# Kernel tuning notes

Hardware: AMD Instinct MI355X
Metric: run time of the kernel (lower is better)

Reference implementation:

```python
import jax, jax.numpy as jnp
import numpy as np

V = 100000      # num nodes
E = 600000      # num edges (even: first half in-edges, second half out-edges)
D_IN = 128
D_OUT = 128
NREL2 = 100     # num_rel * 2
BN_EPS = 1e-5


def ccorr(a, b):
    # circular correlation along last dim: irfft(conj(rfft(a)) * rfft(b), n=d)
    d = a.shape[-1]
    return jnp.fft.irfft(jnp.conj(jnp.fft.rfft(a)) * jnp.fft.rfft(b), n=d).astype(a.dtype)


def setup_inputs() -> dict:
    key = jax.random.key(0)
    ks = jax.random.split(key, 12)
    return {
        "x": jax.random.normal(ks[0], (V, D_IN), dtype=jnp.float32),
        "rel_repr": jax.random.normal(ks[1], (NREL2, D_IN), dtype=jnp.float32),
        "edge_norm": jax.random.uniform(ks[2], (E,), dtype=jnp.float32),
        "in_w": jax.random.normal(ks[3], (D_IN, D_OUT), dtype=jnp.float32) * 0.05,
        "out_w": jax.random.normal(ks[4], (D_IN, D_OUT), dtype=jnp.float32) * 0.05,
        "loop_w": jax.random.normal(ks[5], (D_IN, D_OUT), dtype=jnp.float32) * 0.05,
        "w_rel": jax.random.normal(ks[6], (D_IN, D_OUT), dtype=jnp.float32) * 0.05,
        "loop_rel": jax.random.normal(ks[7], (1, D_IN), dtype=jnp.float32),
        "bias": jnp.zeros((D_OUT,), dtype=jnp.float32),
        "bn_gamma": jnp.ones((D_OUT,), dtype=jnp.float32),
        "bn_beta": jnp.zeros((D_OUT,), dtype=jnp.float32),
        "edge_src": jax.random.randint(ks[8], (E,), 0, V, dtype=jnp.int32),
        "edge_dst": jax.random.randint(ks[9], (E,), 0, V, dtype=jnp.int32),
        "edge_type": jax.random.randint(ks[10], (E,), 0, NREL2, dtype=jnp.int32),
    }


def reference(x, rel_repr, edge_norm, in_w, out_w, loop_w, w_rel, loop_rel,
              bias, bn_gamma, bn_beta, edge_src, edge_dst, edge_type):
    rel = rel_repr  # rel_wt is None (num_base=-1)
    # gather src features per edge and compose with relation embedding (corr)
    edge_data = ccorr(x[edge_src], rel[edge_type])             # [E, D_IN]
    half = edge_data.shape[0] // 2
    msg = jnp.concatenate(
        [edge_data[:half] @ in_w, edge_data[half:] @ out_w], axis=0
    ) * edge_norm[:, None]                                     # [E, D_OUT]
    # scatter-sum into destination nodes
    agg = jax.ops.segment_sum(msg, edge_dst, num_segments=V)   # [V, D_OUT]
    # self-loop term
    loop = ccorr(x, jnp.broadcast_to(loop_rel, x.shape)) @ loop_w
    h = (agg + loop) / 3.0 + bias
    # BatchNorm1d (training mode: batch stats, biased variance)
    mean = h.mean(axis=0)
    var = h.var(axis=0)
    h = (h - mean) * jax.lax.rsqrt(var + BN_EPS) * bn_gamma + bn_beta
    # act is identity; ltr=True -> project relations
    return h, rel @ w_rel
```

## Files before the change

### kernel.cpp

```cpp
#include <hip/hip_runtime.h>
#include <hip/hip_bf16.h>

#define D 128
constexpr int V_N    = 100000;
constexpr int E_N    = 600000;
constexpr int HALF_E = E_N / 2;
constexpr int NREL2  = 100;
constexpr int NBUCK  = 2 * NREL2;
constexpr float BN_EPS_F = 1e-5f;

constexpr int CHUNK  = 4096;
constexpr int NCHUNK = (E_N + CHUNK - 1) / CHUNK;

typedef short bf16x8  __attribute__((ext_vector_type(8)));
typedef float f32x16  __attribute__((ext_vector_type(16)));
typedef float f32x4v  __attribute__((ext_vector_type(4)));

constexpr size_t M_RSV    = 201ull * D * D * 4;
constexpr size_t M_OFF    = 0;
constexpr size_t HIST_OFF = 201ull * D * D * 2;
constexpr size_t COFF_OFF = HIST_OFF + (size_t)NBUCK * NCHUNK * 4;
constexpr size_t SS_OFF   = M_RSV;
constexpr size_t SD_OFF   = SS_OFF + (size_t)E_N * 4;
constexpr size_t SN_OFF   = SD_OFF + (size_t)E_N * 4;
constexpr size_t ZERO_OFF = SN_OFF + (size_t)E_N * 4;
constexpr size_t CNT_OFF  = ZERO_OFF;
constexpr size_t CS_OFF   = ZERO_OFF + 1024;
constexpr size_t CQ_OFF   = CS_OFF + 512;
constexpr size_t ZERO_BYTES = 2048;
constexpr size_t ST_OFF   = ZERO_OFF + ZERO_BYTES;

constexpr size_t MT_BYTES  = 201ull * D * D * 2;
constexpr size_t P_SS_OFF  = MT_BYTES;
constexpr size_t P_SD_OFF  = P_SS_OFF + (size_t)E_N * 4;
constexpr size_t P_SN_OFF  = P_SD_OFF + (size_t)E_N * 4;
constexpr size_t P_AGG_OFF = P_SN_OFF + (size_t)E_N * 4;
constexpr size_t AGG_BYTES = (size_t)V_N * D * 2;
constexpr size_t P_HIST_OFF = P_AGG_OFF;
constexpr size_t P_COFF_OFF = P_HIST_OFF + (size_t)NBUCK * NCHUNK * 4;
constexpr size_t P_CS_OFF  = P_AGG_OFF + AGG_BYTES;
constexpr size_t P_CQ_OFF  = P_CS_OFF + 512;
constexpr size_t P_CNT_OFF = P_CQ_OFF + 512;
constexpr size_t P_ST_OFF  = P_CNT_OFF + 1024;
constexpr size_t WS_NEED_PK = P_ST_OFF + 1024;

__device__ inline unsigned short f2bf(float f) {
    __hip_bfloat16 h = __float2bfloat16(f);
    return __builtin_bit_cast(unsigned short, h);
}
__device__ inline float bf2f(unsigned short u) {
    return __uint_as_float(((unsigned)u) << 16);
}

__device__ inline int bucket_of(int e, const int* __restrict__ etype) {
    return etype[e] + (e < HALF_E ? 0 : NREL2);
}

__global__ __launch_bounds__(256) void k_hist_chunk(const int* __restrict__ etype,
                                                    int* __restrict__ hist) {
    __shared__ int h[NBUCK];
    for (int i = threadIdx.x; i < NBUCK; i += 256) h[i] = 0;
    __syncthreads();
    int c = blockIdx.x;
    int e0 = c * CHUNK;
#pragma unroll
    for (int r = 0; r < CHUNK / 256; r++) {
        int e = e0 + r * 256 + threadIdx.x;
        if (e < E_N) atomicAdd(&h[bucket_of(e, etype)], 1);
    }
    __syncthreads();
    for (int b = threadIdx.x; b < NBUCK; b += 256) hist[b * NCHUNK + c] = h[b];
}

__global__ void k_scan_bucket(const int* __restrict__ hist, int* __restrict__ chunkoff,
                              int* __restrict__ counts) {
    int b = blockIdx.x, lane = threadIdx.x;
    int acc = 0;
    for (int base = 0; base < NCHUNK; base += 64) {
        int c = base + lane;
        int v = (c < NCHUNK) ? hist[b * NCHUNK + c] : 0;
        int s = v;
#pragma unroll
        for (int off = 1; off < 64; off <<= 1) {
            int t = __shfl(s, lane - off, 64);
            if (lane >= off) s += t;
        }
        if (c < NCHUNK) chunkoff[b * NCHUNK + c] = acc + (s - v);
        acc += __shfl(s, 63, 64);
    }
    if (lane == 0) counts[b] = acc;
}

__global__ void k_scan(const int* __restrict__ counts, int* __restrict__ starts) {
    __shared__ int s[256];
    int i = threadIdx.x;
    int v = (i < NBUCK) ? counts[i] : 0;
    s[i] = v;
    __syncthreads();
    for (int off = 1; off < 256; off <<= 1) {
        int t = (i >= off) ? s[i - off] : 0;
        __syncthreads();
        s[i] += t;
        __syncthreads();
    }
    if (i < NBUCK) starts[i] = s[i] - v;
    if (i == 255) starts[NBUCK] = s[255];
}

__global__ __launch_bounds__(256) void k_scatter2(
    const int* __restrict__ src, const int* __restrict__ dst,
    const float* __restrict__ norm, const int* __restrict__ etype,
    const int* __restrict__ starts, const int* __restrict__ chunkoff,
    int* __restrict__ ssrc, int* __restrict__ sdst, float* __restrict__ snorm) {
    __shared__ int h[NBUCK];
    __shared__ int sbase[NBUCK];
    int c = blockIdx.x;
    for (int b = threadIdx.x; b < NBUCK; b += 256) {
        h[b] = 0;
        sbase[b] = starts[b] + chunkoff[b * NCHUNK + c];
    }
    __syncthreads();
    int e0 = c * CHUNK;
#pragma unroll
    for (int r = 0; r < CHUNK / 256; r++) {
        int e = e0 + r * 256 + threadIdx.x;
        if (e < E_N) {
            int b = bucket_of(e, etype);
            int rank = atomicAdd(&h[b], 1);
            int p = sbase[b] + rank;
            ssrc[p] = src[e]; sdst[p] = dst[e]; snorm[p] = norm[e];
        }
    }
}

__global__ void k_build_M(const float* __restrict__ rel, const float* __restrict__ in_w,
                          const float* __restrict__ out_w, const float* __restrict__ loop_rel,
                          const float* __restrict__ loop_w, ushort* __restrict__ MT) {
    extern __shared__ float smem[];
    float* sW = smem;
    float* sR = smem + D * D;
    int b = blockIdx.x;
    const float* r = (b < NREL2) ? rel + (size_t)b * D
                   : (b < NBUCK) ? rel + (size_t)(b - NREL2) * D : loop_rel;
    const float* W = (b < NREL2) ? in_w : (b < NBUCK) ? out_w : loop_w;
    for (int i = threadIdx.x; i < D * D; i += blockDim.x) sW[i] = W[i];
    for (int i = threadIdx.x; i < D; i += blockDim.x) { float v = r[i]; sR[i] = v; sR[i + D] = v; }
    __syncthreads();
    int o  = threadIdx.x & 127;
    int jg = threadIdx.x >> 7;
    ushort* MTb = MT + (size_t)b * (D * D);
    for (int pass = 0; pass < 4; pass++) {
        int jbase = jg * 64 + pass * 16;
        float acc[16];
#pragma unroll
        for (int t = 0; t < 16; t++) acc[t] = 0.f;
        for (int k = 0; k < D; k++) {
            float w = sW[k * D + o];
#pragma unroll
            for (int t = 0; t < 16; t++) acc[t] += sR[jbase + t + k] * w;
        }
#pragma unroll
        for (int t = 0; t < 16; t++) MTb[(size_t)o * D + jbase + t] = f2bf(acc[t]);
    }
}

__global__ void k_relw(const float* __restrict__ rel, const float* __restrict__ w_rel,
                       float* __restrict__ out2) {
    int rr = blockIdx.x, o = threadIdx.x;
    float acc = 0.f;
    for (int k = 0; k < D; k++) acc += rel[rr * D + k] * w_rel[k * D + o];
    out2[rr * D + o] = acc;
}

constexpr int BPB = 8;

__global__ __launch_bounds__(256) void k_edge_pk(
    const float* __restrict__ x, const ushort* __restrict__ MT,
    const int* __restrict__ starts, const int* __restrict__ ssrc,
    const int* __restrict__ sdst, const float* __restrict__ snorm,
    ushort* __restrict__ agg) {
    int wid  = threadIdx.x >> 6, lane = threadIdx.x & 63;
    int l31  = lane & 31, l5 = lane >> 5;
    int bucket = blockIdx.x / BPB;
    int sib    = (blockIdx.x % BPB) * 2 + (wid >> 1);
    int oh     = wid & 1;
    int bstart = starts[bucket], bend = starts[bucket + 1];
    const ushort* MTb = MT + (size_t)bucket * (D * D);
    int c0 = oh * 64 + 2 * l31;
    bf16x8 B0[8], B1[8];
#pragma unroll
    for (int kc = 0; kc < 8; kc++) {
        B0[kc] = *(const bf16x8*)&MTb[(size_t)c0 * D + kc * 16 + l5 * 8];
        B1[kc] = *(const bf16x8*)&MTb[(size_t)(c0 + 1) * D + kc * 16 + l5 * 8];
    }
    for (int tbase = bstart + sib * 32; tbase < bend; tbase += BPB * 2 * 32) {
        int nv = bend - tbase; if (nv > 32) nv = 32;
        int sr = ssrc[tbase + (l31 < nv ? l31 : 0)];
        const float* xr = x + (size_t)sr * D + l5 * 8;
        bf16x8 A[8];
#pragma unroll
        for (int kc = 0; kc < 8; kc++) {
            f32x4v v0 = *(const f32x4v*)(xr + kc * 16);
            f32x4v v1 = *(const f32x4v*)(xr + kc * 16 + 4);
            union { bf16x8 v; ushort u[8]; } t;
            t.u[0] = f2bf(v0[0]); t.u[1] = f2bf(v0[1]); t.u[2] = f2bf(v0[2]); t.u[3] = f2bf(v0[3]);
            t.u[4] = f2bf(v1[0]); t.u[5] = f2bf(v1[1]); t.u[6] = f2bf(v1[2]); t.u[7] = f2bf(v1[3]);
            A[kc] = t.v;
        }
        f32x16 C0, C1;
#pragma unroll
        for (int i = 0; i < 16; i++) { C0[i] = 0.f; C1[i] = 0.f; }
#pragma unroll
        for (int kc = 0; kc < 8; kc++) {
            C0 = __builtin_amdgcn_mfma_f32_32x32x16_bf16(A[kc], B0[kc], C0, 0, 0, 0);
            C1 = __builtin_amdgcn_mfma_f32_32x32x16_bf16(A[kc], B1[kc], C1, 0, 0, 0);
        }
#pragma unroll
        for (int r = 0; r < 16; r++) {
            int rw = (r & 3) + 8 * (r >> 2) + 4 * l5;
            if (rw < nv) {
                float nm = snorm[tbase + rw];
                int   dv = sdst[tbase + rw];
                union { ushort u[2]; unsigned int w; } p;
                p.u[0] = f2bf(C0[r] * nm);
                p.u[1] = f2bf(C1[r] * nm);
                ushort* ap = agg + (size_t)dv * D + c0;
                asm volatile("global_atomic_pk_add_bf16 %0, %1, off"
                             :: "v"(ap), "v"(p.w) : "memory");
            }
        }
    }
}

__global__ __launch_bounds__(256) void k_edge(
    const float* __restrict__ x, const ushort* __restrict__ MT,
    const int* __restrict__ starts, const int* __restrict__ ssrc,
    const int* __restrict__ sdst, const float* __restrict__ snorm,
    float* __restrict__ out) {
    int wid  = threadIdx.x >> 6, lane = threadIdx.x & 63;
    int l31  = lane & 31, l5 = lane >> 5;
    int bucket = blockIdx.x / BPB;
    int sib    = (blockIdx.x % BPB) * 2 + (wid >> 1);
    int oh     = wid & 1;
    int bstart = starts[bucket], bend = starts[bucket + 1];
    const ushort* MTb = MT + (size_t)bucket * (D * D);
    int ocol0 = oh * 64 + l31, ocol1 = oh * 64 + 32 + l31;
    bf16x8 B0[8], B1[8];
#pragma unroll
    for (int kc = 0; kc < 8; kc++) {
        B0[kc] = *(const bf16x8*)&MTb[(size_t)ocol0 * D + kc * 16 + l5 * 8];
        B1[kc] = *(const bf16x8*)&MTb[(size_t)ocol1 * D + kc * 16 + l5 * 8];
    }
    for (int tbase = bstart + sib * 32; tbase < bend; tbase += BPB * 2 * 32) {
        int nv = bend - tbase; if (nv > 32) nv = 32;
        int sr = ssrc[tbase + (l31 < nv ? l31 : 0)];
        const float* xr = x + (size_t)sr * D + l5 * 8;
        bf16x8 A[8];
#pragma unroll
        for (int kc = 0; kc < 8; kc++) {
            f32x4v v0 = *(const f32x4v*)(xr + kc * 16);
            f32x4v v1 = *(const f32x4v*)(xr + kc * 16 + 4);
            union { bf16x8 v; ushort u[8]; } t;
            t.u[0] = f2bf(v0[0]); t.u[1] = f2bf(v0[1]); t.u[2] = f2bf(v0[2]); t.u[3] = f2bf(v0[3]);
            t.u[4] = f2bf(v1[0]); t.u[5] = f2bf(v1[1]); t.u[6] = f2bf(v1[2]); t.u[7] = f2bf(v1[3]);
            A[kc] = t.v;
        }
        f32x16 C0, C1;
#pragma unroll
        for (int i = 0; i < 16; i++) { C0[i] = 0.f; C1[i] = 0.f; }
#pragma unroll
        for (int kc = 0; kc < 8; kc++) {
            C0 = __builtin_amdgcn_mfma_f32_32x32x16_bf16(A[kc], B0[kc], C0, 0, 0, 0);
            C1 = __builtin_amdgcn_mfma_f32_32x32x16_bf16(A[kc], B1[kc], C1, 0, 0, 0);
        }
#pragma unroll
        for (int r = 0; r < 16; r++) {
            int rw = (r & 3) + 8 * (r >> 2) + 4 * l5;
            if (rw < nv) {
                float nm = snorm[tbase + rw];
                int   dv = sdst[tbase + rw];
                float* op = out + (size_t)dv * D;
                atomicAdd(op + ocol0, C0[r] * nm);
                atomicAdd(op + ocol1, C1[r] * nm);
            }
        }
    }
}

constexpr int LOOP_GRID = 400;
__global__ __launch_bounds__(256) void k_loop_pk(
    const float* __restrict__ x, const ushort* __restrict__ MT,
    const float* __restrict__ bias, const ushort* __restrict__ agg,
    float* __restrict__ out, float* __restrict__ colsum, float* __restrict__ colsq) {
    int wid = threadIdx.x >> 6, lane = threadIdx.x & 63;
    int l31 = lane & 31, l5 = lane >> 5;
    int oh  = wid & 1;
    int strm = blockIdx.x * 2 + (wid >> 1);
    const int NSTR = LOOP_GRID * 2;
    const ushort* MTb = MT + (size_t)NBUCK * (D * D);
    int ocol0 = oh * 64 + l31, ocol1 = oh * 64 + 32 + l31;
    bf16x8 B0[8], B1[8];
#pragma unroll
    for (int kc = 0; kc < 8; kc++) {
        B0[kc] = *(const bf16x8*)&MTb[(size_t)ocol0 * D + kc * 16 + l5 * 8];
        B1[kc] = *(const bf16x8*)&MTb[(size_t)ocol1 * D + kc * 16 + l5 * 8];
    }
    float b0 = bias[ocol0], b1 = bias[ocol1];
    float ps0 = 0.f, pq0 = 0.f, ps1 = 0.f, pq1 = 0.f;
    const int NT = V_N / 32;
    for (int tile = strm; tile < NT; tile += NSTR) {
        int tbase = tile * 32;
        const float* xr = x + (size_t)(tbase + l31) * D + l5 * 8;
        bf16x8 A[8];
#pragma unroll
        for (int kc = 0; kc < 8; kc++) {
            f32x4v v0 = *(const f32x4v*)(xr + kc * 16);
            f32x4v v1 = *(const f32x4v*)(xr + kc * 16 + 4);
            union { bf16x8 v; ushort u[8]; } t;
            t.u[0] = f2bf(v0[0]); t.u[1] = f2bf(v0[1]); t.u[2] = f2bf(v0[2]); t.u[3] = f2bf(v0[3]);
            t.u[4] = f2bf(v1[0]); t.u[5] = f2bf(v1[1]); t.u[6] = f2bf(v1[2]); t.u[7] = f2bf(v1[3]);
            A[kc] = t.v;
        }
        f32x16 C0, C1;
#pragma unroll
        for (int i = 0; i < 16; i++) { C0[i] = 0.f; C1[i] = 0.f; }
#pragma unroll
        for (int kc = 0; kc < 8; kc++) {
            C0 = __builtin_amdgcn_mfma_f32_32x32x16_bf16(A[kc], B0[kc], C0, 0, 0, 0);
            C1 = __builtin_amdgcn_mfma_f32_32x32x16_bf16(A[kc], B1[kc], C1, 0, 0, 0);
        }
#pragma unroll
        for (int r = 0; r < 16; r++) {
            int rw = (r & 3) + 8 * (r >> 2) + 4 * l5;
            size_t i0 = (size_t)(tbase + rw) * D + ocol0;
            size_t i1 = (size_t)(tbase + rw) * D + ocol1;
            float h0 = (bf2f(agg[i0]) + C0[r]) * (1.f / 3.f) + b0;
            float h1 = (bf2f(agg[i1]) + C1[r]) * (1.f / 3.f) + b1;
            out[i0] = h0; out[i1] = h1;
            ps0 += h0; pq0 += h0 * h0;
            ps1 += h1; pq1 += h1 * h1;
        }
    }
    atomicAdd(&colsum[ocol0], ps0); atomicAdd(&colsq[ocol0], pq0);
    atomicAdd(&colsum[ocol1], ps1); atomicAdd(&colsq[ocol1], pq1);
}

__global__ __launch_bounds__(256) void k_loop(
    const float* __restrict__ x, const ushort* __restrict__ MT,
    const float* __restrict__ bias, float* __restrict__ out,
    float* __restrict__ colsum, float* __restrict__ colsq) {
    int wid = threadIdx.x >> 6, lane = threadIdx.x & 63;
    int l31 = lane & 31, l5 = lane >> 5;
    int oh  = wid & 1;
    int strm = blockIdx.x * 2 + (wid >> 1);
    const int NSTR = LOOP_GRID * 2;
    const ushort* MTb = MT + (size_t)NBUCK * (D * D);
    int ocol0 = oh * 64 + l31, ocol1 = oh * 64 + 32 + l31;
    bf16x8 B0[8], B1[8];
#pragma unroll
    for (int kc = 0; kc < 8; kc++) {
        B0[kc] = *(const bf16x8*)&MTb[(size_t)ocol0 * D + kc * 16 + l5 * 8];
        B1[kc] = *(const bf16x8*)&MTb[(size_t)ocol1 * D + kc * 16 + l5 * 8];
    }
    float b0 = bias[ocol0], b1 = bias[ocol1];
    float ps0 = 0.f, pq0 = 0.f, ps1 = 0.f, pq1 = 0.f;
    const int NT = V_N / 32;
    for (int tile = strm; tile < NT; tile += NSTR) {
        int tbase = tile * 32;
        const float* xr = x + (size_t)(tbase + l31) * D + l5 * 8;
        bf16x8 A[8];
#pragma unroll
        for (int kc = 0; kc < 8; kc++) {
            f32x4v v0 = *(const f32x4v*)(xr + kc * 16);
            f32x4v v1 = *(const f32x4v*)(xr + kc * 16 + 4);
            union { bf16x8 v; ushort u[8]; } t;
            t.u[0] = f2bf(v0[0]); t.u[1] = f2bf(v0[1]); t.u[2] = f2bf(v0[2]); t.u[3] = f2bf(v0[3]);
            t.u[4] = f2bf(v1[0]); t.u[5] = f2bf(v1[1]); t.u[6] = f2bf(v1[2]); t.u[7] = f2bf(v1[3]);
            A[kc] = t.v;
        }
        f32x16 C0, C1;
#pragma unroll
        for (int i = 0; i < 16; i++) { C0[i] = 0.f; C1[i] = 0.f; }
#pragma unroll
        for (int kc = 0; kc < 8; kc++) {
            C0 = __builtin_amdgcn_mfma_f32_32x32x16_bf16(A[kc], B0[kc], C0, 0, 0, 0);
            C1 = __builtin_amdgcn_mfma_f32_32x32x16_bf16(A[kc], B1[kc], C1, 0, 0, 0);
        }
#pragma unroll
        for (int r = 0; r < 16; r++) {
            int rw = (r & 3) + 8 * (r >> 2) + 4 * l5;
            size_t i0 = (size_t)(tbase + rw) * D + ocol0;
            size_t i1 = (size_t)(tbase + rw) * D + ocol1;
            float h0 = (out[i0] + C0[r]) * (1.f / 3.f) + b0;
            float h1 = (out[i1] + C1[r]) * (1.f / 3.f) + b1;
            out[i0] = h0; out[i1] = h1;
            ps0 += h0; pq0 += h0 * h0;
            ps1 += h1; pq1 += h1 * h1;
        }
    }
    atomicAdd(&colsum[ocol0], ps0); atomicAdd(&colsq[ocol0], pq0);
    atomicAdd(&colsum[ocol1], ps1); atomicAdd(&colsq[ocol1], pq1);
}

__global__ void k_bn(float* __restrict__ out, const float* __restrict__ colsum,
                     const float* __restrict__ colsq, const float* __restrict__ gamma,
                     const float* __restrict__ beta) {
    const size_t N4 = (size_t)V_N * D / 4;
    size_t stride = (size_t)gridDim.x * blockDim.x;
    for (size_t q = (size_t)blockIdx.x * blockDim.x + threadIdx.x; q < N4; q += stride) {
        int c4 = (int)(q & 31);
        float4 s  = *(const float4*)&colsum[c4 * 4];
        float4 sq = *(const float4*)&colsq[c4 * 4];
        float4 g  = *(const float4*)&gamma[c4 * 4];
        float4 be = *(const float4*)&beta[c4 * 4];
        float4 h  = *(float4*)&out[q * 4];
        const float inv = 1.f / (float)V_N;
        float m0 = s.x * inv, m1 = s.y * inv, m2 = s.z * inv, m3 = s.w * inv;
        float r0 = rsqrtf(sq.x * inv - m0 * m0 + BN_EPS_F);
        float r1 = rsqrtf(sq.y * inv - m1 * m1 + BN_EPS_F);
        float r2 = rsqrtf(sq.z * inv - m2 * m2 + BN_EPS_F);
        float r3 = rsqrtf(sq.w * inv - m3 * m3 + BN_EPS_F);
        h.x = (h.x - m0) * r0 * g.x + be.x;
        h.y = (h.y - m1) * r1 * g.y + be.y;
        h.z = (h.z - m2) * r2 * g.z + be.z;
        h.w = (h.w - m3) * r3 * g.w + be.w;
        *(float4*)&out[q * 4] = h;
    }
}

extern "C" void kernel_launch(void* const* d_in, const int* in_sizes, int n_in,
                              void* d_out, int out_size, void* d_ws, size_t ws_size,
                              hipStream_t stream) {
    const float* x        = (const float*)d_in[0];
    const float* rel      = (const float*)d_in[1];
    const float* enorm    = (const float*)d_in[2];
    const float* in_w     = (const float*)d_in[3];
    const float* out_w    = (const float*)d_in[4];
    const float* loop_w   = (const float*)d_in[5];
    const float* w_rel    = (const float*)d_in[6];
    const float* loop_rel = (const float*)d_in[7];
    const float* bias     = (const float*)d_in[8];
    const float* gamma    = (const float*)d_in[9];
    const float* beta     = (const float*)d_in[10];
    const int*   esrc     = (const int*)d_in[11];
    const int*   edst     = (const int*)d_in[12];
    const int*   etype    = (const int*)d_in[13];
    float* out = (float*)d_out;
    char*  ws  = (char*)d_ws;

    int gM = 201, smem = (D * D + 256) * sizeof(float);

    if (ws_size >= WS_NEED_PK) {
        ushort* MT       = (ushort*)(ws + 0);
        int*    ssrc     = (int*)(ws + P_SS_OFF);
        int*    sdst     = (int*)(ws + P_SD_OFF);
        float*  snorm    = (float*)(ws + P_SN_OFF);
        ushort* aggbf    = (ushort*)(ws + P_AGG_OFF);
        int*    hist     = (int*)(ws + P_HIST_OFF);
        int*    chunkoff = (int*)(ws + P_COFF_OFF);
        float*  colsum   = (float*)(ws + P_CS_OFF);
        float*  colsq    = (float*)(ws + P_CQ_OFF);
        int*    counts   = (int*)(ws + P_CNT_OFF);
        int*    starts   = (int*)(ws + P_ST_OFF);

        hipMemsetAsync(ws + P_CS_OFF, 0, 1024, stream);

        k_hist_chunk<<<NCHUNK, 256, 0, stream>>>(etype, hist);
        k_scan_bucket<<<NBUCK, 64, 0, stream>>>(hist, chunkoff, counts);
        k_scan<<<1, 256, 0, stream>>>(counts, starts);
        k_scatter2<<<NCHUNK, 256, 0, stream>>>(esrc, edst, enorm, etype, starts, chunkoff,
                                               ssrc, sdst, snorm);
        hipMemsetAsync(ws + P_AGG_OFF, 0, AGG_BYTES, stream);

        k_build_M<<<gM, 256, smem, stream>>>(rel, in_w, out_w, loop_rel, loop_w, MT);
        k_relw<<<NREL2, D, 0, stream>>>(rel, w_rel, out + (size_t)V_N * D);

        k_edge_pk<<<NBUCK * BPB, 256, 0, stream>>>(x, MT, starts, ssrc, sdst, snorm, aggbf);
        k_loop_pk<<<LOOP_GRID, 256, 0, stream>>>(x, MT, bias, aggbf, out, colsum, colsq);
        k_bn<<<2048, 256, 0, stream>>>(out, colsum, colsq, gamma, beta);
    } else {
        ushort* MT       = (ushort*)(ws + M_OFF);
        int*    hist     = (int*)(ws + HIST_OFF);
        int*    chunkoff = (int*)(ws + COFF_OFF);
        int*    ssrc     = (int*)(ws + SS_OFF);
        int*    sdst     = (int*)(ws + SD_OFF);
        float*  snorm    = (float*)(ws + SN_OFF);
        int*    counts   = (int*)(ws + CNT_OFF);
        float*  colsum   = (float*)(ws + CS_OFF);
        float*  colsq    = (float*)(ws + CQ_OFF);
        int*    starts   = (int*)(ws + ST_OFF);

        hipMemsetAsync(out, 0, (size_t)V_N * D * sizeof(float), stream);
        hipMemsetAsync(ws + ZERO_OFF, 0, ZERO_BYTES, stream);

        k_hist_chunk<<<NCHUNK, 256, 0, stream>>>(etype, hist);
        k_scan_bucket<<<NBUCK, 64, 0, stream>>>(hist, chunkoff, counts);
        k_scan<<<1, 256, 0, stream>>>(counts, starts);
        k_scatter2<<<NCHUNK, 256, 0, stream>>>(esrc, edst, enorm, etype, starts, chunkoff,
                                               ssrc, sdst, snorm);

        k_build_M<<<gM, 256, smem, stream>>>(rel, in_w, out_w, loop_rel, loop_w, MT);
        k_relw<<<NREL2, D, 0, stream>>>(rel, w_rel, out + (size_t)V_N * D);

        k_edge<<<NBUCK * BPB, 256, 0, stream>>>(x, MT, starts, ssrc, sdst, snorm, out);
        k_loop<<<LOOP_GRID, 256, 0, stream>>>(x, MT, bias, out, colsum, colsq);
        k_bn<<<2048, 256, 0, stream>>>(out, colsum, colsq, gamma, beta);
    }
}
```

Before: 562.3 us.

## Pre-convert x to bf16 and use per-block partial BN stats

```diff
diff --git a/kernel.cpp b/kernel.cpp
--- a/kernel.cpp
+++ b/kernel.cpp
@@ -15,20 +15,7 @@
 typedef short bf16x8  __attribute__((ext_vector_type(8)));
 typedef float f32x16  __attribute__((ext_vector_type(16)));
 typedef float f32x4v  __attribute__((ext_vector_type(4)));
-
-constexpr size_t M_RSV    = 201ull * D * D * 4;
-constexpr size_t M_OFF    = 0;
-constexpr size_t HIST_OFF = 201ull * D * D * 2;
-constexpr size_t COFF_OFF = HIST_OFF + (size_t)NBUCK * NCHUNK * 4;
-constexpr size_t SS_OFF   = M_RSV;
-constexpr size_t SD_OFF   = SS_OFF + (size_t)E_N * 4;
-constexpr size_t SN_OFF   = SD_OFF + (size_t)E_N * 4;
-constexpr size_t ZERO_OFF = SN_OFF + (size_t)E_N * 4;
-constexpr size_t CNT_OFF  = ZERO_OFF;
-constexpr size_t CS_OFF   = ZERO_OFF + 1024;
-constexpr size_t CQ_OFF   = CS_OFF + 512;
-constexpr size_t ZERO_BYTES = 2048;
-constexpr size_t ST_OFF   = ZERO_OFF + ZERO_BYTES;
+typedef unsigned int uint32;
 
 constexpr size_t MT_BYTES  = 201ull * D * D * 2;
 constexpr size_t P_SS_OFF  = MT_BYTES;
@@ -44,12 +31,18 @@
 constexpr size_t P_ST_OFF  = P_CNT_OFF + 1024;
 constexpr size_t WS_NEED_PK = P_ST_OFF + 1024;
 
+constexpr int LOOP_GRID2 = 782;
+constexpr size_t P2_XBF  = (WS_NEED_PK + 255) & ~(size_t)255;
+constexpr size_t P2_PSUM = P2_XBF + AGG_BYTES;
+constexpr size_t P2_PSQ  = P2_PSUM + 128ull * LOOP_GRID2 * 4;
+constexpr size_t WS_NEED2 = P2_PSQ + 128ull * LOOP_GRID2 * 4;
+
 __device__ inline unsigned short f2bf(float f) {
     __hip_bfloat16 h = __float2bfloat16(f);
     return __builtin_bit_cast(unsigned short, h);
 }
-__device__ inline float bf2f(unsigned short u) {
-    return __uint_as_float(((unsigned)u) << 16);
+__device__ inline float bf2f(unsigned int u) {
+    return __uint_as_float(u << 16);
 }
 
 __device__ inline int bucket_of(int e, const int* __restrict__ etype) {
@@ -131,6 +124,19 @@
             ssrc[p] = src[e]; sdst[p] = dst[e]; snorm[p] = norm[e];
         }
     }
+}
+
+__global__ __launch_bounds__(256) void k_xbf(const float* __restrict__ x,
+                                             ushort* __restrict__ xbf) {
+    const int N8 = V_N * D / 8;
+    int i = blockIdx.x * 256 + threadIdx.x;
+    if (i >= N8) return;
+    f32x4v v0 = *(const f32x4v*)&x[(size_t)i * 8];
+    f32x4v v1 = *(const f32x4v*)&x[(size_t)i * 8 + 4];
+    union { ushort u[8]; uint4 q; } t;
+    t.u[0] = f2bf(v0[0]); t.u[1] = f2bf(v0[1]); t.u[2] = f2bf(v0[2]); t.u[3] = f2bf(v0[3]);
+    t.u[4] = f2bf(v1[0]); t.u[5] = f2bf(v1[1]); t.u[6] = f2bf(v1[2]); t.u[7] = f2bf(v1[3]);
+    *(uint4*)&xbf[(size_t)i * 8] = t.q;
 }
 
 __global__ void k_build_M(const float* __restrict__ rel, const float* __restrict__ in_w,
@@ -173,6 +179,134 @@
 }
 
 constexpr int BPB = 8;
+
+__global__ __launch_bounds__(256) void k_edge_pkb(
+    const ushort* __restrict__ xbf, const ushort* __restrict__ MT,
+    const int* __restrict__ starts, const int* __restrict__ ssrc,
+    const int* __restrict__ sdst, const float* __restrict__ snorm,
+    ushort* __restrict__ agg) {
+    int wid  = threadIdx.x >> 6, lane = threadIdx.x & 63;
+    int l31  = lane & 31, l5 = lane >> 5;
+    int bucket = blockIdx.x / BPB;
+    int sib    = (blockIdx.x % BPB) * 2 + (wid >> 1);
+    int oh     = wid & 1;
+    int bstart = starts[bucket], bend = starts[bucket + 1];
+    const ushort* MTb = MT + (size_t)bucket * (D * D);
+    int c0 = oh * 64 + 2 * l31;
+    bf16x8 B0[8], B1[8];
+#pragma unroll
+    for (int kc = 0; kc < 8; kc++) {
+        B0[kc] = *(const bf16x8*)&MTb[(size_t)c0 * D + kc * 16 + l5 * 8];
+        B1[kc] = *(const bf16x8*)&MTb[(size_t)(c0 + 1) * D + kc * 16 + l5 * 8];
+    }
+    for (int tbase = bstart + sib * 32; tbase < bend; tbase += BPB * 2 * 32) {
+        int nv = bend - tbase; if (nv > 32) nv = 32;
+        int sr = ssrc[tbase + (l31 < nv ? l31 : 0)];
+        const ushort* xr = xbf + (size_t)sr * D + l5 * 8;
+        bf16x8 A[8];
+#pragma unroll
+        for (int kc = 0; kc < 8; kc++) A[kc] = *(const bf16x8*)(xr + kc * 16);
+        f32x16 C0, C1;
+#pragma unroll
+        for (int i = 0; i < 16; i++) { C0[i] = 0.f; C1[i] = 0.f; }
+#pragma unroll
+        for (int kc = 0; kc < 8; kc++) {
+            C0 = __builtin_amdgcn_mfma_f32_32x32x16_bf16(A[kc], B0[kc], C0, 0, 0, 0);
+            C1 = __builtin_amdgcn_mfma_f32_32x32x16_bf16(A[kc], B1[kc], C1, 0, 0, 0);
+        }
+#pragma unroll
+        for (int r = 0; r < 16; r++) {
+            int rw = (r & 3) + 8 * (r >> 2) + 4 * l5;
+            if (rw < nv) {
+                float nm = snorm[tbase + rw];
+                int   dv = sdst[tbase + rw];
+                union { ushort u[2]; unsigned int w; } p;
+                p.u[0] = f2bf(C0[r] * nm);
+                p.u[1] = f2bf(C1[r] * nm);
+                ushort* ap = agg + (size_t)dv * D + c0;
+                asm volatile("global_atomic_pk_add_bf16 %0, %1, off"
+                             :: "v"(ap), "v"(p.w) : "memory");
+            }
+        }
+    }
+}
+
+__global__ __launch_bounds__(256) void k_loop_nb(
+    const ushort* __restrict__ xbf, const ushort* __restrict__ MT,
+    const float* __restrict__ bias, const ushort* __restrict__ agg,
+    float* __restrict__ out, float* __restrict__ psum, float* __restrict__ psq) {
+    __shared__ float lsum[128], lsq[128];
+    if (threadIdx.x < 128) { lsum[threadIdx.x] = 0.f; lsq[threadIdx.x] = 0.f; }
+    int wid = threadIdx.x >> 6, lane = threadIdx.x & 63;
+    int l31 = lane & 31, l5 = lane >> 5;
+    int oh  = wid & 1;
+    int strm = blockIdx.x * 2 + (wid >> 1);
+    const int NSTR = LOOP_GRID2 * 2;
+    const ushort* MTb = MT + (size_t)NBUCK * (D * D);
+    int ocol0 = oh * 64 + l31, ocol1 = oh * 64 + 32 + l31;
+    bf16x8 B0[8], B1[8];
+#pragma unroll
+    for (int kc = 0; kc < 8; kc++) {
+        B0[kc] = *(const bf16x8*)&MTb[(size_t)ocol0 * D + kc * 16 + l5 * 8];
+        B1[kc] = *(const bf16x8*)&MTb[(size_t)ocol1 * D + kc * 16 + l5 * 8];
+    }
+    float b0 = bias[ocol0], b1 = bias[ocol1];
+    float ps0 = 0.f, pq0 = 0.f, ps1 = 0.f, pq1 = 0.f;
+    const int NT = V_N / 32;
+    for (int tile = strm; tile < NT; tile += NSTR) {
+        int tbase = tile * 32;
+        const ushort* xr = xbf + (size_t)(tbase + l31) * D + l5 * 8;
+        bf16x8 A[8];
+#pragma unroll
+        for (int kc = 0; kc < 8; kc++) A[kc] = *(const bf16x8*)(xr + kc * 16);
+        f32x16 C0, C1;
+#pragma unroll
+        for (int i = 0; i < 16; i++) { C0[i] = 0.f; C1[i] = 0.f; }
+#pragma unroll
+        for (int kc = 0; kc < 8; kc++) {
+            C0 = __builtin_amdgcn_mfma_f32_32x32x16_bf16(A[kc], B0[kc], C0, 0, 0, 0);
+            C1 = __builtin_amdgcn_mfma_f32_32x32x16_bf16(A[kc], B1[kc], C1, 0, 0, 0);
+        }
+#pragma unroll
+        for (int r = 0; r < 16; r++) {
+            int rw = (r & 3) + 8 * (r >> 2) + 4 * l5;
+            size_t i0 = (size_t)(tbase + rw) * D + ocol0;
+            size_t i1 = (size_t)(tbase + rw) * D + ocol1;
+            float h0 = (bf2f((uint32)agg[i0]) + C0[r]) * (1.f / 3.f) + b0;
+            float h1 = (bf2f((uint32)agg[i1]) + C1[r]) * (1.f / 3.f) + b1;
+            out[i0] = h0; out[i1] = h1;
+            ps0 += h0; pq0 += h0 * h0;
+            ps1 += h1; pq1 += h1 * h1;
+        }
+    }
+    __syncthreads();
+    atomicAdd(&lsum[ocol0], ps0); atomicAdd(&lsq[ocol0], pq0);
+    atomicAdd(&lsum[ocol1], ps1); atomicAdd(&lsq[ocol1], pq1);
+    __syncthreads();
+    if (threadIdx.x < 128) {
+        psum[(size_t)threadIdx.x * LOOP_GRID2 + blockIdx.x] = lsum[threadIdx.x];
+        psq [(size_t)threadIdx.x * LOOP_GRID2 + blockIdx.x] = lsq [threadIdx.x];
+    }
+}
+
+__global__ __launch_bounds__(256) void k_colreduce(
+    const float* __restrict__ psum, const float* __restrict__ psq,
+    float* __restrict__ colsum, float* __restrict__ colsq) {
+    __shared__ float ls[256], lq[256];
+    int c = blockIdx.x, tid = threadIdx.x;
+    float s = 0.f, q = 0.f;
+    for (int b = tid; b < LOOP_GRID2; b += 256) {
+        s += psum[(size_t)c * LOOP_GRID2 + b];
+        q += psq [(size_t)c * LOOP_GRID2 + b];
+    }
+    ls[tid] = s; lq[tid] = q;
+    __syncthreads();
+    for (int off = 128; off > 0; off >>= 1) {
+        if (tid < off) { ls[tid] += ls[tid + off]; lq[tid] += lq[tid + off]; }
+        __syncthreads();
+    }
+    if (tid == 0) { colsum[c] = ls[0]; colsq[c] = lq[0]; }
+}
 
 __global__ __launch_bounds__(256) void k_edge_pk(
     const float* __restrict__ x, const ushort* __restrict__ MT,
@@ -232,61 +366,6 @@
     }
 }
 
-__global__ __launch_bounds__(256) void k_edge(
-    const float* __restrict__ x, const ushort* __restrict__ MT,
-    const int* __restrict__ starts, const int* __restrict__ ssrc,
-    const int* __restrict__ sdst, const float* __restrict__ snorm,
-    float* __restrict__ out) {
-    int wid  = threadIdx.x >> 6, lane = threadIdx.x & 63;
-    int l31  = lane & 31, l5 = lane >> 5;
-    int bucket = blockIdx.x / BPB;
-    int sib    = (blockIdx.x % BPB) * 2 + (wid >> 1);
-    int oh     = wid & 1;
-    int bstart = starts[bucket], bend = starts[bucket + 1];
-    const ushort* MTb = MT + (size_t)bucket * (D * D);
-    int ocol0 = oh * 64 + l31, ocol1 = oh * 64 + 32 + l31;
-    bf16x8 B0[8], B1[8];
-#pragma unroll
-    for (int kc = 0; kc < 8; kc++) {
-        B0[kc] = *(const bf16x8*)&MTb[(size_t)ocol0 * D + kc * 16 + l5 * 8];
-        B1[kc] = *(const bf16x8*)&MTb[(size_t)ocol1 * D + kc * 16 + l5 * 8];
-    }
-    for (int tbase = bstart + sib * 32; tbase < bend; tbase += BPB * 2 * 32) {
-        int nv = bend - tbase; if (nv > 32) nv = 32;
-        int sr = ssrc[tbase + (l31 < nv ? l31 : 0)];
-        const float* xr = x + (size_t)sr * D + l5 * 8;
-        bf16x8 A[8];
-#pragma unroll
-        for (int kc = 0; kc < 8; kc++) {
-            f32x4v v0 = *(const f32x4v*)(xr + kc * 16);
-            f32x4v v1 = *(const f32x4v*)(xr + kc * 16 + 4);
-            union { bf16x8 v; ushort u[8]; } t;
-            t.u[0] = f2bf(v0[0]); t.u[1] = f2bf(v0[1]); t.u[2] = f2bf(v0[2]); t.u[3] = f2bf(v0[3]);
-            t.u[4] = f2bf(v1[0]); t.u[5] = f2bf(v1[1]); t.u[6] = f2bf(v1[2]); t.u[7] = f2bf(v1[3]);
-            A[kc] = t.v;
-        }
-        f32x16 C0, C1;
-#pragma unroll
-        for (int i = 0; i < 16; i++) { C0[i] = 0.f; C1[i] = 0.f; }
-#pragma unroll
-        for (int kc = 0; kc < 8; kc++) {
-            C0 = __builtin_amdgcn_mfma_f32_32x32x16_bf16(A[kc], B0[kc], C0, 0, 0, 0);
-            C1 = __builtin_amdgcn_mfma_f32_32x32x16_bf16(A[kc], B1[kc], C1, 0, 0, 0);
-        }
-#pragma unroll
-        for (int r = 0; r < 16; r++) {
-            int rw = (r & 3) + 8 * (r >> 2) + 4 * l5;
-            if (rw < nv) {
-                float nm = snorm[tbase + rw];
-                int   dv = sdst[tbase + rw];
-                float* op = out + (size_t)dv * D;
-                atomicAdd(op + ocol0, C0[r] * nm);
-                atomicAdd(op + ocol1, C1[r] * nm);
-            }
-        }
-    }
-}
-
 constexpr int LOOP_GRID = 400;
 __global__ __launch_bounds__(256) void k_loop_pk(
     const float* __restrict__ x, const ushort* __restrict__ MT,
@@ -334,65 +413,8 @@
             int rw = (r & 3) + 8 * (r >> 2) + 4 * l5;
             size_t i0 = (size_t)(tbase + rw) * D + ocol0;
             size_t i1 = (size_t)(tbase + rw) * D + ocol1;
-            float h0 = (bf2f(agg[i0]) + C0[r]) * (1.f / 3.f) + b0;
-            float h1 = (bf2f(agg[i1]) + C1[r]) * (1.f / 3.f) + b1;
-            out[i0] = h0; out[i1] = h1;
-            ps0 += h0; pq0 += h0 * h0;
-            ps1 += h1; pq1 += h1 * h1;
-        }
-    }
-    atomicAdd(&colsum[ocol0], ps0); atomicAdd(&colsq[ocol0], pq0);
-    atomicAdd(&colsum[ocol1], ps1); atomicAdd(&colsq[ocol1], pq1);
-}
-
-__global__ __launch_bounds__(256) void k_loop(
-    const float* __restrict__ x, const ushort* __restrict__ MT,
-    const float* __restrict__ bias, float* __restrict__ out,
-    float* __restrict__ colsum, float* __restrict__ colsq) {
-    int wid = threadIdx.x >> 6, lane = threadIdx.x & 63;
-    int l31 = lane & 31, l5 = lane >> 5;
-    int oh  = wid & 1;
-    int strm = blockIdx.x * 2 + (wid >> 1);
-    const int NSTR = LOOP_GRID * 2;
-    const ushort* MTb = MT + (size_t)NBUCK * (D * D);
-    int ocol0 = oh * 64 + l31, ocol1 = oh * 64 + 32 + l31;
-    bf16x8 B0[8], B1[8];
-#pragma unroll
-    for (int kc = 0; kc < 8; kc++) {
-        B0[kc] = *(const bf16x8*)&MTb[(size_t)ocol0 * D + kc * 16 + l5 * 8];
-        B1[kc] = *(const bf16x8*)&MTb[(size_t)ocol1 * D + kc * 16 + l5 * 8];
-    }
-    float b0 = bias[ocol0], b1 = bias[ocol1];
-    float ps0 = 0.f, pq0 = 0.f, ps1 = 0.f, pq1 = 0.f;
-    const int NT = V_N / 32;
-    for (int tile = strm; tile < NT; tile += NSTR) {
-        int tbase = tile * 32;
-        const float* xr = x + (size_t)(tbase + l31) * D + l5 * 8;
-        bf16x8 A[8];
-#pragma unroll
-        for (int kc = 0; kc < 8; kc++) {
-            f32x4v v0 = *(const f32x4v*)(xr + kc * 16);
-            f32x4v v1 = *(const f32x4v*)(xr + kc * 16 + 4);
-            union { bf16x8 v; ushort u[8]; } t;
-            t.u[0] = f2bf(v0[0]); t.u[1] = f2bf(v0[1]); t.u[2] = f2bf(v0[2]); t.u[3] = f2bf(v0[3]);
-            t.u[4] = f2bf(v1[0]); t.u[5] = f2bf(v1[1]); t.u[6] = f2bf(v1[2]); t.u[7] = f2bf(v1[3]);
-            A[kc] = t.v;
-        }
-        f32x16 C0, C1;
-#pragma unroll
-        for (int i = 0; i < 16; i++) { C0[i] = 0.f; C1[i] = 0.f; }
-#pragma unroll
-        for (int kc = 0; kc < 8; kc++) {
-            C0 = __builtin_amdgcn_mfma_f32_32x32x16_bf16(A[kc], B0[kc], C0, 0, 0, 0);
-            C1 = __builtin_amdgcn_mfma_f32_32x32x16_bf16(A[kc], B1[kc], C1, 0, 0, 0);
-        }
-#pragma unroll
-        for (int r = 0; r < 16; r++) {
-            int rw = (r & 3) + 8 * (r >> 2) + 4 * l5;
-            size_t i0 = (size_t)(tbase + rw) * D + ocol0;
-            size_t i1 = (size_t)(tbase + rw) * D + ocol1;
-            float h0 = (out[i0] + C0[r]) * (1.f / 3.f) + b0;
-            float h1 = (out[i1] + C1[r]) * (1.f / 3.f) + b1;
+            float h0 = (bf2f((uint32)agg[i0]) + C0[r]) * (1.f / 3.f) + b0;
+            float h1 = (bf2f((uint32)agg[i1]) + C1[r]) * (1.f / 3.f) + b1;
             out[i0] = h0; out[i1] = h1;
             ps0 += h0; pq0 += h0 * h0;
             ps1 += h1; pq1 += h1 * h1;
@@ -448,62 +470,44 @@
     float* out = (float*)d_out;
     char*  ws  = (char*)d_ws;
 
-    int gM = 201, smem = (D * D + 256) * sizeof(float);
-
-    if (ws_size >= WS_NEED_PK) {
-        ushort* MT       = (ushort*)(ws + 0);
-        int*    ssrc     = (int*)(ws + P_SS_OFF);
-        int*    sdst     = (int*)(ws + P_SD_OFF);
-        float*  snorm    = (float*)(ws + P_SN_OFF);
-        ushort* aggbf    = (ushort*)(ws + P_AGG_OFF);
-        int*    hist     = (int*)(ws + P_HIST_OFF);
-        int*    chunkoff = (int*)(ws + P_COFF_OFF);
-        float*  colsum   = (float*)(ws + P_CS_OFF);
-        float*  colsq    = (float*)(ws + P_CQ_OFF);
-        int*    counts   = (int*)(ws + P_CNT_OFF);
-        int*    starts   = (int*)(ws + P_ST_OFF);
-
+    const int gM = 201, smem = (D * D + 256) * sizeof(float);
+
+    ushort* MT     = (ushort*)(ws + 0);
+    int*    ssrc   = (int*)(ws + P_SS_OFF);
+    int*    sdst   = (int*)(ws + P_SD_OFF);
+    float*  snorm  = (float*)(ws + P_SN_OFF);
+    ushort* aggbf  = (ushort*)(ws + P_AGG_OFF);
+    int*    hist   = (int*)(ws + P_HIST_OFF);
+    int*    coff   = (int*)(ws + P_COFF_OFF);
+    float*  colsum = (float*)(ws + P_CS_OFF);
+    float*  colsq  = (float*)(ws + P_CQ_OFF);
+    int*    counts = (int*)(ws + P_CNT_OFF);
+    int*    starts = (int*)(ws + P_ST_OFF);
+
+    k_hist_chunk<<<NCHUNK, 256, 0, stream>>>(etype, hist);
+    k_scan_bucket<<<NBUCK, 64, 0, stream>>>(hist, coff, counts);
+    k_scan<<<1, 256, 0, stream>>>(counts, starts);
+    k_scatter2<<<NCHUNK, 256, 0, stream>>>(esrc, edst, enorm, etype, starts, coff,
+                                           ssrc, sdst, snorm);
+    hipMemsetAsync(ws + P_AGG_OFF, 0, AGG_BYTES, stream);
+
+    k_build_M<<<gM, 256, smem, stream>>>(rel, in_w, out_w, loop_rel, loop_w, MT);
+    k_relw<<<NREL2, D, 0, stream>>>(rel, w_rel, out + (size_t)V_N * D);
+
+    if (ws_size >= WS_NEED2) {
+        ushort* xbf  = (ushort*)(ws + P2_XBF);
+        float*  psum = (float*)(ws + P2_PSUM);
+        float*  psq  = (float*)(ws + P2_PSQ);
+
+        k_xbf<<<(V_N * D / 8 + 255) / 256, 256, 0, stream>>>(x, xbf);
+        k_edge_pkb<<<NBUCK * BPB, 256, 0, stream>>>(xbf, MT, starts, ssrc, sdst, snorm, aggbf);
+        k_loop_nb<<<LOOP_GRID2, 256, 0, stream>>>(xbf, MT, bias, aggbf, out, psum, psq);
+        k_colreduce<<<128, 256, 0, stream>>>(psum, psq, colsum, colsq);
+        k_bn<<<2048, 256, 0, stream>>>(out, colsum, colsq, gamma, beta);
+    } else {
         hipMemsetAsync(ws + P_CS_OFF, 0, 1024, stream);
-
-        k_hist_chunk<<<NCHUNK, 256, 0, stream>>>(etype, hist);
-        k_scan_bucket<<<NBUCK, 64, 0, stream>>>(hist, chunkoff, counts);
-        k_scan<<<1, 256, 0, stream>>>(counts, starts);
-        k_scatter2<<<NCHUNK, 256, 0, stream>>>(esrc, edst, enorm, etype, starts, chunkoff,
-                                               ssrc, sdst, snorm);
-        hipMemsetAsync(ws + P_AGG_OFF, 0, AGG_BYTES, stream);
-
-        k_build_M<<<gM, 256, smem, stream>>>(rel, in_w, out_w, loop_rel, loop_w, MT);
-        k_relw<<<NREL2, D, 0, stream>>>(rel, w_rel, out + (size_t)V_N * D);
-
         k_edge_pk<<<NBUCK * BPB, 256, 0, stream>>>(x, MT, starts, ssrc, sdst, snorm, aggbf);
         k_loop_pk<<<LOOP_GRID, 256, 0, stream>>>(x, MT, bias, aggbf, out, colsum, colsq);
         k_bn<<<2048, 256, 0, stream>>>(out, colsum, colsq, gamma, beta);
-    } else {
-        ushort* MT       = (ushort*)(ws + M_OFF);
-        int*    hist     = (int*)(ws + HIST_OFF);
-        int*    chunkoff = (int*)(ws + COFF_OFF);
-        int*    ssrc     = (int*)(ws + SS_OFF);
-        int*    sdst     = (int*)(ws + SD_OFF);
-        float*  snorm    = (float*)(ws + SN_OFF);
-        int*    counts   = (int*)(ws + CNT_OFF);
-        float*  colsum   = (float*)(ws + CS_OFF);
-        float*  colsq    = (float*)(ws + CQ_OFF);
-        int*    starts   = (int*)(ws + ST_OFF);
-
-        hipMemsetAsync(out, 0, (size_t)V_N * D * sizeof(float), stream);
-        hipMemsetAsync(ws + ZERO_OFF, 0, ZERO_BYTES, stream);
-
-        k_hist_chunk<<<NCHUNK, 256, 0, stream>>>(etype, hist);
-        k_scan_bucket<<<NBUCK, 64, 0, stream>>>(hist, chunkoff, counts);
-        k_scan<<<1, 256, 0, stream>>>(counts, starts);
-        k_scatter2<<<NCHUNK, 256, 0, stream>>>(esrc, edst, enorm, etype, starts, chunkoff,
-                                               ssrc, sdst, snorm);
-
-        k_build_M<<<gM, 256, smem, stream>>>(rel, in_w, out_w, loop_rel, loop_w, MT);
-        k_relw<<<NREL2, D, 0, stream>>>(rel, w_rel, out + (size_t)V_N * D);
-
-        k_edge<<<NBUCK * BPB, 256, 0, stream>>>(x, MT, starts, ssrc, sdst, snorm, out);
-        k_loop<<<LOOP_GRID, 256, 0, stream>>>(x, MT, bias, out, colsum, colsq);
-        k_bn<<<2048, 256, 0, stream>>>(out, colsum, colsq, gamma, beta);
-    }
-}
+    }
+}
```

New measurement: 458.6 us. -18.4%, faster.
